# Performance work log

Measured on AMD Instinct MI355X. Metric: run time of the kernel, lower is better.

The kernel has to match this reference:

```python
import jax, jax.numpy as jnp
import numpy as np
from jax import lax

D_MODEL = 1024
D_INNER = 2048
B = 8
T = 2048
INIT_ALPHA_BIAS = 2.0


def setup_inputs() -> dict:
    key = jax.random.key(0)
    ks = jax.random.split(key, 6)
    def xavier(k, shape):
        fan_in, fan_out = shape[1], shape[0]
        lim = float(np.sqrt(6.0 / (fan_in + fan_out)))
        return jax.random.uniform(k, shape, jnp.float32, -lim, lim)
    return {
        "x": jax.random.normal(ks[0], (B, T, D_MODEL), jnp.float32),
        "h0": jnp.zeros((B, D_INNER), jnp.float32),
        "W_in": xavier(ks[1], (D_INNER, D_MODEL)),
        "W_alpha": xavier(ks[2], (D_INNER, D_INNER)),
        "b_alpha": jnp.full((D_INNER,), INIT_ALPHA_BIAS, jnp.float32),
        "W_v": xavier(ks[3], (D_INNER, D_INNER)),
        "b_v": jnp.zeros((D_INNER,), jnp.float32),
        "W_out": xavier(ks[4], (D_MODEL, D_INNER)),
    }


def reference(x, h0, W_in, W_alpha, b_alpha, W_v, b_v, W_out):
    # in_proj + silu pre-activation: [B,T,D_inner]
    x_proj = jax.nn.silu(jnp.einsum('btd,id->bti', x, W_in))
    # time-major for the scan: [T,B,D_inner]
    xr = jnp.transpose(x_proj, (1, 0, 2))
    # precompute gate and value for all steps (big GEMMs)
    alpha = jax.nn.sigmoid(jnp.einsum('tbd,ed->tbe', xr, W_alpha) + b_alpha)
    v = jnp.einsum('tbd,ed->tbe', xr, W_v) + b_v

    def step(h, av):
        a, vt = av
        h_new = a * h + (1.0 - a) * vt  # decay-gated update
        out_t = h_new * jax.nn.silu(h_new)  # self-gating
        return h_new, out_t

    h_final, outs = lax.scan(step, h0, (alpha, v))  # outs: [T,B,D_inner]
    # out_proj back to model dim, batch-major: [B,T,D_model]
    output = jnp.einsum('tbe,de->btd', outs, W_out)
    return output, h_final
```

## Files before the change

kernel.cpp:

```cpp
#include <hip/hip_runtime.h>
#include <cstdint>
#include <cstddef>

typedef unsigned short u16;
typedef unsigned int   u32;

#define D_MODEL 1024
#define D_INNER 2048
#define BATCH   8
#define TSEQ    2048
#define MROWS   (BATCH*TSEQ)
#define CHUNK   32
#define NCHUNK  (TSEQ/CHUNK)
#define EDIM    (BATCH*D_INNER)

typedef float  f32x4  __attribute__((ext_vector_type(4)));
typedef __bf16 bf16x8 __attribute__((ext_vector_type(8)));
typedef short  s16x8  __attribute__((ext_vector_type(8)));

__device__ __forceinline__ float bf2f(u16 u){ return __builtin_bit_cast(float, (u32)u << 16); }
__device__ __forceinline__ u16 f2bf(float f){
  u32 u = __builtin_bit_cast(u32, f);
  u += 0x7fffu + ((u >> 16) & 1u);
  return (u16)(u >> 16);
}
__device__ __forceinline__ float sigm(float x){ return 1.0f/(1.0f + __expf(-x)); }

__device__ __forceinline__ void gld16(const u16* g, u16* l){
  __builtin_amdgcn_global_load_lds((const __attribute__((address_space(1))) void*)g,
                                   (__attribute__((address_space(3))) void*)l, 16, 0, 0);
}

__device__ __forceinline__ s16x8 cvt8(const float* s){
  float4 u0 = *(const float4*)s;
  float4 u1 = *(const float4*)(s + 4);
  s16x8 p;
  p[0]=(short)f2bf(u0.x); p[1]=(short)f2bf(u0.y);
  p[2]=(short)f2bf(u0.z); p[3]=(short)f2bf(u0.w);
  p[4]=(short)f2bf(u1.x); p[5]=(short)f2bf(u1.y);
  p[6]=(short)f2bf(u1.z); p[7]=(short)f2bf(u1.w);
  return p;
}

#define LOADA(AF, MH) \
  _Pragma("unroll") \
  for (int mf = 0; mf < 4; ++mf){ \
    AF[mf][0] = *(const s16x8*)(As + (wr*128 + (MH)*64 + mf*16 + l15)*128 + csw); \
    AF[mf][1] = *(const s16x8*)(As + (wr*128 + (MH)*64 + mf*16 + l15)*128 + (csw^64)); \
  }
#define LOADB(BF, NH) \
  _Pragma("unroll") \
  for (int nf = 0; nf < 2; ++nf){ \
    BF[nf][0] = *(const s16x8*)(Bs + (wc*64 + (NH)*32 + nf*16 + l15)*128 + csw); \
    BF[nf][1] = *(const s16x8*)(Bs + (wc*64 + (NH)*32 + nf*16 + l15)*128 + (csw^64)); \
  }
#define MFMAQ(AF, BF, MH, NH) \
  __builtin_amdgcn_s_setprio(1); \
  _Pragma("unroll") \
  for (int mf = 0; mf < 4; ++mf) \
    _Pragma("unroll") \
    for (int nf = 0; nf < 2; ++nf) \
      _Pragma("unroll") \
      for (int ks = 0; ks < 2; ++ks) \
        acc[(MH)*4+mf][(NH)*2+nf] = __builtin_amdgcn_mfma_f32_16x16x32_bf16( \
            __builtin_bit_cast(bf16x8, AF[mf][ks]), \
            __builtin_bit_cast(bf16x8, BF[nf][ks]), \
            acc[(MH)*4+mf][(NH)*2+nf], 0, 0, 0); \
  __builtin_amdgcn_s_setprio(0);

template<int MODE, int K, int N>
__global__ __launch_bounds__(512, 2) void gemm256(
    const u16* __restrict__ A, const u16* __restrict__ Bt,
    const float* __restrict__ bias, const float* __restrict__ bias2,
    void* __restrict__ Cout, void* __restrict__ Cout2)
{
  __shared__ __align__(16) u16 sAB[2][2][16384];
  constexpr int NT = K/64;
  const int tid = threadIdx.x;
  const int w = tid >> 6, lane = tid & 63;
  const int wr = w >> 2, wc = w & 3;
  const int l15 = lane & 15, kg = lane >> 4;
  const int bm = blockIdx.x, bn = blockIdx.y;

  const int st_row  = w*8 + (lane>>3);
  const int st_cole = ((lane&7) ^ (lane>>3)) << 3;
  const size_t a_base = (size_t)(bm*256)*K + st_cole;
  const size_t b_base = (size_t)(bn*256)*K + st_cole;

  auto stageA = [&](int buf, int kt, int upper){
    u16* dst = &sAB[0][buf][upper*8192 + w*512];
    #pragma unroll
    for (int i = 0; i < 2; ++i)
      gld16(A + a_base + (size_t)(upper*128 + i*64 + st_row)*K + kt*64, dst + i*4096);
  };
  auto stageB = [&](int buf, int kt, int upper){
    u16* dst = &sAB[1][buf][upper*8192 + w*512];
    #pragma unroll
    for (int i = 0; i < 2; ++i)
      gld16(Bt + b_base + (size_t)(upper*128 + i*64 + st_row)*K + kt*64, dst + i*4096);
  };

  const int csw = (kg*16) ^ ((l15&7)<<4);

  f32x4 acc[8][4] = {};

  stageA(0,0,0); stageB(0,0,0); stageA(0,0,1); stageB(0,0,1);
  asm volatile("s_waitcnt vmcnt(0)" ::: "memory");
  __builtin_amdgcn_s_barrier();

  for (int t = 0; t < NT; ++t){
    const char* As = (const char*)&sAB[0][t&1][0];
    const char* Bs = (const char*)&sAB[1][t&1][0];
    const int nb = (t+1)&1;
    const bool more = (t < NT-1);
    s16x8 af[4][2], bf0[2][2], bf1[2][2];

    LOADA(af, 0)
    LOADB(bf0, 0)
    if (more){ stageA(nb, t+1, 0); stageA(nb, t+1, 1); }
    __builtin_amdgcn_s_barrier();
    MFMAQ(af, bf0, 0, 0)
    __builtin_amdgcn_s_barrier();

    LOADB(bf1, 1)
    if (more){ stageB(nb, t+1, 0); stageB(nb, t+1, 1); }
    __builtin_amdgcn_s_barrier();
    MFMAQ(af, bf1, 0, 1)
    __builtin_amdgcn_s_barrier();

    LOADA(af, 1)
    __builtin_amdgcn_s_barrier();
    MFMAQ(af, bf1, 1, 1)
    __builtin_amdgcn_s_barrier();

    asm volatile("s_waitcnt vmcnt(0)" ::: "memory");
    __builtin_amdgcn_s_barrier();
    MFMAQ(af, bf0, 1, 0)
    __builtin_amdgcn_s_barrier();
  }

  #pragma unroll
  for (int mi = 0; mi < 8; ++mi){
    #pragma unroll
    for (int ni = 0; ni < 4; ++ni){
      #pragma unroll
      for (int r = 0; r < 4; ++r){
        const int row = bm*256 + wr*128 + mi*16 + kg*4 + r;
        const int col = bn*256 + wc*64 + ni*16 + l15;
        float val = acc[mi][ni][r];
        if constexpr (MODE == 0){
          val = val * sigm(val);
          ((u16*)Cout)[(size_t)row*N + col] = f2bf(val);
        } else if constexpr (MODE == 3){
          const int orow = (row & 7)*TSEQ + (row >> 3);
          ((float*)Cout)[(size_t)orow*N + col] = val;
        } else if constexpr (MODE == 4){
          if (col < D_INNER){
            val = sigm(val + bias[col]);
            ((u16*)Cout)[(size_t)row*D_INNER + col] = f2bf(val);
          } else {
            val = val + bias2[col - D_INNER];
            ((u16*)Cout2)[(size_t)row*D_INNER + (col - D_INNER)] = f2bf(val);
          }
        }
      }
    }
  }
}

template<int MODE, int K, int N, bool BA, bool BB>
__global__ __launch_bounds__(256) void gemm_bt(
    const void* __restrict__ Ap, const void* __restrict__ Bp,
    const float* __restrict__ bias, void* __restrict__ Cout)
{
  __shared__ __align__(16) u16 sA[128*32];
  __shared__ __align__(16) u16 sB[128*32];
  const int tid = threadIdx.x;
  const int bm = blockIdx.x, bn = blockIdx.y;
  const int w = tid >> 6, lane = tid & 63;
  const int wr = w >> 1, wc = w & 1;
  const int l15 = lane & 15, kg = lane >> 4;
  const int r0   = tid >> 2;
  const int koff = (tid & 3) * 8;

  int ga[2];
  #pragma unroll
  for (int i = 0; i < 2; ++i){
    int mc = bm*128 + r0 + i*64;
    if (MODE == 0)      ga[i] = (mc & 7) * TSEQ + (mc >> 3);
    else if (MODE == 3) ga[i] = (mc & (TSEQ-1)) * BATCH + (mc >> 11);
    else                ga[i] = mc;
  }
  const u16*   Abf = (const u16*)Ap;
  const float* Af  = (const float*)Ap;
  const u16*   Bbf = (const u16*)Bp;
  const float* Bf  = (const float*)Bp;
  u16* la[2] = { sA + w*512, sA + 2048 + w*512 };
  u16* lb[2] = { sB + w*512, sB + 2048 + w*512 };
  u16* ldsA = sA + tid*8;
  u16* ldsB = sB + tid*8;
  const int gb[2] = { bn*128 + r0, bn*128 + r0 + 64 };

  f32x4 acc[4][4] = {};
  for (int kt = 0; kt < K/32; ++kt){
    __syncthreads();
    if constexpr (BA){
      gld16(Abf + (size_t)ga[0]*K + koff + kt*32, la[0]);
      gld16(Abf + (size_t)ga[1]*K + koff + kt*32, la[1]);
    } else {
      #pragma unroll
      for (int i = 0; i < 2; ++i)
        *(s16x8*)(ldsA + i*2048) = cvt8(Af + (size_t)ga[i]*K + koff + kt*32);
    }
    if constexpr (BB){
      gld16(Bbf + (size_t)gb[0]*K + koff + kt*32, lb[0]);
      gld16(Bbf + (size_t)gb[1]*K + koff + kt*32, lb[1]);
    } else {
      #pragma unroll
      for (int i = 0; i < 2; ++i)
        *(s16x8*)(ldsB + i*2048) = cvt8(Bf + (size_t)gb[i]*K + koff + kt*32);
    }
    __syncthreads();

    s16x8 af[4], bfr[4];
    #pragma unroll
    for (int m = 0; m < 4; ++m)
      af[m] = *(const s16x8*)(sA + (wr*64 + m*16 + l15)*32 + kg*8);
    #pragma unroll
    for (int n = 0; n < 4; ++n)
      bfr[n] = *(const s16x8*)(sB + (wc*64 + n*16 + l15)*32 + kg*8);
    #pragma unroll
    for (int m = 0; m < 4; ++m)
      #pragma unroll
      for (int n = 0; n < 4; ++n)
        acc[m][n] = __builtin_amdgcn_mfma_f32_16x16x32_bf16(
            __builtin_bit_cast(bf16x8, af[m]),
            __builtin_bit_cast(bf16x8, bfr[n]),
            acc[m][n], 0, 0, 0);
  }
  #pragma unroll
  for (int m = 0; m < 4; ++m)
    #pragma unroll
    for (int n = 0; n < 4; ++n)
      #pragma unroll
      for (int r = 0; r < 4; ++r){
        const int row = bm*128 + wr*64 + m*16 + kg*4 + r;
        const int col = bn*128 + wc*64 + n*16 + l15;
        float val = acc[m][n][r];
        if constexpr (MODE == 0){
          val = val * sigm(val);
          ((u16*)Cout)[(size_t)row*N + col] = f2bf(val);
        } else if constexpr (MODE == 1){
          val = sigm(val + bias[col]);
          ((u16*)Cout)[(size_t)row*N + col] = f2bf(val);
        } else if constexpr (MODE == 2){
          val = val + bias[col];
          ((u16*)Cout)[(size_t)row*N + col] = f2bf(val);
        } else {
          ((float*)Cout)[(size_t)row*N + col] = val;
        }
      }
}

__global__ __launch_bounds__(256) void scan_pass1(
    const u16* __restrict__ alpha, const u16* __restrict__ v,
    float* __restrict__ P, float* __restrict__ H)
{
  const int e = blockIdx.x*256 + threadIdx.x;
  const int c = blockIdx.y;
  const size_t base = (size_t)c*CHUNK*EDIM + e;
  float p = 1.f, h = 0.f;
  #pragma unroll 8
  for (int t = 0; t < CHUNK; ++t){
    float a  = bf2f(alpha[base + (size_t)t*EDIM]);
    float vv = bf2f(v[base + (size_t)t*EDIM]);
    p *= a;
    h = a*h + (1.f - a)*vv;
  }
  P[(size_t)c*EDIM + e] = p;
  H[(size_t)c*EDIM + e] = h;
}

__global__ __launch_bounds__(256) void scan_pass2(
    const float* __restrict__ P, const float* __restrict__ H,
    const float* __restrict__ h0, float* __restrict__ hstart,
    float* __restrict__ hfinal)
{
  const int e = blockIdx.x*256 + threadIdx.x;
  float hs = h0[e];
  for (int c = 0; c < NCHUNK; ++c){
    hstart[(size_t)c*EDIM + e] = hs;
    hs = P[(size_t)c*EDIM + e]*hs + H[(size_t)c*EDIM + e];
  }
  hfinal[e] = hs;
}

__global__ __launch_bounds__(256) void scan_pass3(
    const u16* __restrict__ alpha, const u16* __restrict__ v,
    const float* __restrict__ hstart, u16* __restrict__ outs)
{
  const int e = blockIdx.x*256 + threadIdx.x;
  const int c = blockIdx.y;
  const size_t base = (size_t)c*CHUNK*EDIM + e;
  float h = hstart[(size_t)c*EDIM + e];
  #pragma unroll 8
  for (int t = 0; t < CHUNK; ++t){
    float a  = bf2f(alpha[base + (size_t)t*EDIM]);
    float vv = bf2f(v[base + (size_t)t*EDIM]);
    h = a*h + (1.f - a)*vv;
    float o = h*h*sigm(h);
    outs[base + (size_t)t*EDIM] = f2bf(o);
  }
}

__global__ __launch_bounds__(256) void cvt_bf16(
    const float* __restrict__ src, u16* __restrict__ dst, int n4)
{
  const int i = blockIdx.x*256 + threadIdx.x;
  if (i >= n4) return;
  const float4 f = ((const float4*)src)[i];
  u32 w0 = (u32)f2bf(f.x) | ((u32)f2bf(f.y) << 16);
  u32 w1 = (u32)f2bf(f.z) | ((u32)f2bf(f.w) << 16);
  ((uint2*)dst)[i] = make_uint2(w0, w1);
}

__global__ __launch_bounds__(256) void cvt_x_tm(
    const float* __restrict__ src, u16* __restrict__ dst)
{
  const int i = blockIdx.x*256 + threadIdx.x;
  const int d4  = i & 255;
  const int rin = i >> 8;
  const int b = rin >> 11, tt = rin & (TSEQ-1);
  const int rout = tt*BATCH + b;
  const float4 f = ((const float4*)src)[i];
  u32 w0 = (u32)f2bf(f.x) | ((u32)f2bf(f.y) << 16);
  u32 w1 = (u32)f2bf(f.z) | ((u32)f2bf(f.w) << 16);
  ((uint2*)dst)[(size_t)rout*256 + d4] = make_uint2(w0, w1);
}

extern "C" void kernel_launch(void* const* d_in, const int* in_sizes, int n_in,
                              void* d_out, int out_size, void* d_ws, size_t ws_size,
                              hipStream_t stream)
{
  const float* x     = (const float*)d_in[0];
  const float* h0    = (const float*)d_in[1];
  const float* W_in  = (const float*)d_in[2];
  const float* W_al  = (const float*)d_in[3];
  const float* b_al  = (const float*)d_in[4];
  const float* W_v   = (const float*)d_in[5];
  const float* b_v   = (const float*)d_in[6];
  const float* W_out = (const float*)d_in[7];

  float* out  = (float*)d_out;
  float* hfin = out + (size_t)MROWS*D_MODEL;

  const size_t SZ_ACT = (size_t)MROWS*D_INNER*2;
  const size_t SZ_ST  = (size_t)NCHUNK*EDIM*4;
  const size_t SZ_WI  = (size_t)D_INNER*D_MODEL*2;
  const size_t SZ_WA  = (size_t)D_INNER*D_INNER*2;
  const size_t need_min  = 3*SZ_ACT + 3*SZ_ST;
  const size_t need_fast = need_min + 2*SZ_WI + 2*SZ_WA + 8192;

  if (ws_size < need_min) return;

  char* ws = (char*)d_ws;
  auto carve = [&](size_t bytes){
    char* p = ws; ws += (bytes + 255) & ~(size_t)255; return p;
  };
  u16* xp   = (u16*)carve(SZ_ACT);
  u16* alp  = (u16*)carve(SZ_ACT);
  u16* vv   = (u16*)carve(SZ_ACT);
  float* P  = (float*)carve(SZ_ST);
  float* H  = (float*)carve(SZ_ST);
  float* hs = (float*)carve(SZ_ST);

  const dim3 gScan(EDIM/256, NCHUNK);

  auto cvt = [&](const float* s, u16* d, size_t n){
    int n4 = (int)(n/4);
    cvt_bf16<<<(n4+255)/256, 256, 0, stream>>>(s, d, n4);
  };

  if (ws_size >= need_fast){
    u16* wib = (u16*)carve(SZ_WI);
    u16* wab = (u16*)carve(SZ_WA);
    u16* wvb = (u16*)carve(SZ_WA);
    u16* wob = (u16*)carve(SZ_WI);
    u16* xb  = alp;

    cvt_x_tm<<<(MROWS*D_MODEL/4)/256, 256, 0, stream>>>(x, xb);
    cvt(W_in,  wib, (size_t)D_INNER*D_MODEL);
    cvt(W_al,  wab, (size_t)D_INNER*D_INNER);
    cvt(W_v,   wvb, (size_t)D_INNER*D_INNER);
    cvt(W_out, wob, (size_t)D_MODEL*D_INNER);

    gemm256<0, D_MODEL, D_INNER><<<dim3(MROWS/256, D_INNER/256), 512, 0, stream>>>(
        xb, wib, nullptr, nullptr, xp, nullptr);
    gemm256<4, D_INNER, 2*D_INNER><<<dim3(MROWS/256, 2*D_INNER/256), 512, 0, stream>>>(
        xp, wab, b_al, b_v, alp, vv);

    scan_pass1<<<gScan, 256, 0, stream>>>(alp, vv, P, H);
    scan_pass2<<<EDIM/256, 256, 0, stream>>>(P, H, h0, hs, hfin);
    scan_pass3<<<gScan, 256, 0, stream>>>(alp, vv, hs, vv);

    gemm256<3, D_INNER, D_MODEL><<<dim3(MROWS/256, D_MODEL/256), 512, 0, stream>>>(
        vv, wob, nullptr, nullptr, out, nullptr);
  } else {
    const dim3 gBig(MROWS/128, D_INNER/128);
    const dim3 gOut(MROWS/128, D_MODEL/128);
    gemm_bt<0, D_MODEL, D_INNER, false, false><<<gBig, 256, 0, stream>>>(x,  W_in, nullptr, xp);
    gemm_bt<1, D_INNER, D_INNER, true,  false><<<gBig, 256, 0, stream>>>(xp, W_al, b_al,    alp);
    gemm_bt<2, D_INNER, D_INNER, true,  false><<<gBig, 256, 0, stream>>>(xp, W_v,  b_v,     vv);

    scan_pass1<<<gScan, 256, 0, stream>>>(alp, vv, P, H);
    scan_pass2<<<EDIM/256, 256, 0, stream>>>(P, H, h0, hs, hfin);
    scan_pass3<<<gScan, 256, 0, stream>>>(alp, vv, hs, vv);

    gemm_bt<3, D_INNER, D_MODEL, true, false><<<gOut, 256, 0, stream>>>(vv, W_out, nullptr, out);
  }
}
```

Baseline: 547.5 us.

## Reorder GEMM tile staging and use partial vmcnt waits for finer overlap

```diff
diff --git a/kernel.cpp b/kernel.cpp
--- a/kernel.cpp
+++ b/kernel.cpp
@@ -82,30 +82,35 @@
   const int l15 = lane & 15, kg = lane >> 4;
   const int bm = blockIdx.x, bn = blockIdx.y;
 
-  const int st_row  = w*8 + (lane>>3);
-  const int st_cole = ((lane&7) ^ (lane>>3)) << 3;
+  const int st_rw   = lane >> 3;
+  const int st_cole = ((lane&7) ^ st_rw) << 3;
   const size_t a_base = (size_t)(bm*256)*K + st_cole;
   const size_t b_base = (size_t)(bn*256)*K + st_cole;
 
-  auto stageA = [&](int buf, int kt, int upper){
-    u16* dst = &sAB[0][buf][upper*8192 + w*512];
-    #pragma unroll
-    for (int i = 0; i < 2; ++i)
-      gld16(A + a_base + (size_t)(upper*128 + i*64 + st_row)*K + kt*64, dst + i*4096);
+  auto stageA = [&](int buf, int kt, int set){
+    u16* dst = &sAB[0][buf][set*4096 + w*512];
+    #pragma unroll
+    for (int i = 0; i < 2; ++i){
+      const int row = set*64 + i*128 + w*8 + st_rw;
+      gld16(A + a_base + (size_t)row*K + kt*64, dst + i*8192);
+    }
   };
-  auto stageB = [&](int buf, int kt, int upper){
-    u16* dst = &sAB[1][buf][upper*8192 + w*512];
-    #pragma unroll
-    for (int i = 0; i < 2; ++i)
-      gld16(Bt + b_base + (size_t)(upper*128 + i*64 + st_row)*K + kt*64, dst + i*4096);
+  auto stageB = [&](int buf, int kt, int set){
+    #pragma unroll
+    for (int i = 0; i < 2; ++i){
+      const int g = i*64 + w*8;
+      const int rowbase = (g>>5)*64 + set*32 + (g&31);
+      gld16(Bt + b_base + (size_t)(rowbase + st_rw)*K + kt*64,
+            &sAB[1][buf][rowbase*64]);
+    }
   };
 
   const int csw = (kg*16) ^ ((l15&7)<<4);
 
   f32x4 acc[8][4] = {};
 
-  stageA(0,0,0); stageB(0,0,0); stageA(0,0,1); stageB(0,0,1);
-  asm volatile("s_waitcnt vmcnt(0)" ::: "memory");
+  stageB(0,0,0); stageA(0,0,0); stageB(0,0,1); stageA(0,0,1);
+  asm volatile("s_waitcnt vmcnt(4)" ::: "memory");
   __builtin_amdgcn_s_barrier();
 
   for (int t = 0; t < NT; ++t){
@@ -117,23 +122,36 @@
 
     LOADA(af, 0)
     LOADB(bf0, 0)
-    if (more){ stageA(nb, t+1, 0); stageA(nb, t+1, 1); }
+    if (more){
+      stageB(nb, t+1, 0); stageA(nb, t+1, 0);
+      asm volatile("s_waitcnt vmcnt(6)" ::: "memory");
+    } else {
+      asm volatile("s_waitcnt vmcnt(2)" ::: "memory");
+    }
     __builtin_amdgcn_s_barrier();
     MFMAQ(af, bf0, 0, 0)
     __builtin_amdgcn_s_barrier();
 
     LOADB(bf1, 1)
-    if (more){ stageB(nb, t+1, 0); stageB(nb, t+1, 1); }
+    if (more){
+      stageB(nb, t+1, 1);
+      asm volatile("s_waitcnt vmcnt(6)" ::: "memory");
+    } else {
+      asm volatile("s_waitcnt vmcnt(0)" ::: "memory");
+    }
     __builtin_amdgcn_s_barrier();
     MFMAQ(af, bf1, 0, 1)
     __builtin_amdgcn_s_barrier();
 
     LOADA(af, 1)
+    if (more){ stageA(nb, t+1, 1); }
     __builtin_amdgcn_s_barrier();
     MFMAQ(af, bf1, 1, 1)
     __builtin_amdgcn_s_barrier();
 
-    asm volatile("s_waitcnt vmcnt(0)" ::: "memory");
+    if (more){
+      asm volatile("s_waitcnt vmcnt(4)" ::: "memory");
+    }
     __builtin_amdgcn_s_barrier();
     MFMAQ(af, bf0, 1, 0)
     __builtin_amdgcn_s_barrier();
```

Measured after the change: 538.9 us. Within noise of the previous version (-1.6%).

## Restructure GEMM mainloop into 4-stage K=32 pipeline with register double-buffering

Applied to the files above, without the earlier changes.

```diff
diff --git a/kernel.cpp b/kernel.cpp
--- a/kernel.cpp
+++ b/kernel.cpp
@@ -42,31 +42,41 @@
   return p;
 }
 
-#define LOADA(AF, MH) \
+#define READR(AF, BF, RBUF) { \
+  const char* As_ = (const char*)&sAB[0][RBUF][0]; \
+  const char* Bs_ = (const char*)&sAB[1][RBUF][0]; \
   _Pragma("unroll") \
-  for (int mf = 0; mf < 4; ++mf){ \
-    AF[mf][0] = *(const s16x8*)(As + (wr*128 + (MH)*64 + mf*16 + l15)*128 + csw); \
-    AF[mf][1] = *(const s16x8*)(As + (wr*128 + (MH)*64 + mf*16 + l15)*128 + (csw^64)); \
-  }
-#define LOADB(BF, NH) \
+  for (int mi = 0; mi < 8; ++mi) \
+    AF[mi] = *(const s16x8*)(As_ + aoff + mi*1024); \
   _Pragma("unroll") \
-  for (int nf = 0; nf < 2; ++nf){ \
-    BF[nf][0] = *(const s16x8*)(Bs + (wc*64 + (NH)*32 + nf*16 + l15)*128 + csw); \
-    BF[nf][1] = *(const s16x8*)(Bs + (wc*64 + (NH)*32 + nf*16 + l15)*128 + (csw^64)); \
-  }
-#define MFMAQ(AF, BF, MH, NH) \
+  for (int ni = 0; ni < 4; ++ni) \
+    BF[ni] = *(const s16x8*)(Bs_ + boff + ni*1024); \
+}
+
+#define MFMAC(AF, BF) \
   __builtin_amdgcn_s_setprio(1); \
   _Pragma("unroll") \
-  for (int mf = 0; mf < 4; ++mf) \
+  for (int mi = 0; mi < 8; ++mi) \
     _Pragma("unroll") \
-    for (int nf = 0; nf < 2; ++nf) \
-      _Pragma("unroll") \
-      for (int ks = 0; ks < 2; ++ks) \
-        acc[(MH)*4+mf][(NH)*2+nf] = __builtin_amdgcn_mfma_f32_16x16x32_bf16( \
-            __builtin_bit_cast(bf16x8, AF[mf][ks]), \
-            __builtin_bit_cast(bf16x8, BF[nf][ks]), \
-            acc[(MH)*4+mf][(NH)*2+nf], 0, 0, 0); \
+    for (int ni = 0; ni < 4; ++ni) \
+      acc[mi][ni] = __builtin_amdgcn_mfma_f32_16x16x32_bf16( \
+          __builtin_bit_cast(bf16x8, AF[mi]), \
+          __builtin_bit_cast(bf16x8, BF[ni]), \
+          acc[mi][ni], 0, 0, 0); \
   __builtin_amdgcn_s_setprio(0);
+
+#define ITER(J, AC, BC, AN, BN, RBUF, SBUF) { \
+  if ((J) < NT-2) { asm volatile("s_waitcnt vmcnt(4)" ::: "memory"); } \
+  else            { asm volatile("s_waitcnt vmcnt(0)" ::: "memory"); } \
+  __builtin_amdgcn_s_barrier(); \
+  if ((J)+1 < NT) READR(AN, BN, RBUF) \
+  if ((J)+3 < NT) stage(SBUF, (J)+3); \
+  __builtin_amdgcn_sched_barrier(0); \
+  if ((J)+1 < NT) { asm volatile("s_waitcnt lgkmcnt(12)" ::: "memory"); } \
+  else            { asm volatile("s_waitcnt lgkmcnt(0)" ::: "memory"); } \
+  __builtin_amdgcn_sched_barrier(0); \
+  MFMAC(AC, BC) \
+}
 
 template<int MODE, int K, int N>
 __global__ __launch_bounds__(512, 2) void gemm256(
@@ -74,69 +84,44 @@
     const float* __restrict__ bias, const float* __restrict__ bias2,
     void* __restrict__ Cout, void* __restrict__ Cout2)
 {
-  __shared__ __align__(16) u16 sAB[2][2][16384];
-  constexpr int NT = K/64;
+  __shared__ __align__(16) u16 sAB[2][4][8192];
+  constexpr int NT = K/32;
   const int tid = threadIdx.x;
   const int w = tid >> 6, lane = tid & 63;
   const int wr = w >> 2, wc = w & 3;
   const int l15 = lane & 15, kg = lane >> 4;
   const int bm = blockIdx.x, bn = blockIdx.y;
 
-  const int st_row  = w*8 + (lane>>3);
-  const int st_cole = ((lane&7) ^ (lane>>3)) << 3;
-  const size_t a_base = (size_t)(bm*256)*K + st_cole;
-  const size_t b_base = (size_t)(bn*256)*K + st_cole;
-
-  auto stageA = [&](int buf, int kt, int upper){
-    u16* dst = &sAB[0][buf][upper*8192 + w*512];
-    #pragma unroll
-    for (int i = 0; i < 2; ++i)
-      gld16(A + a_base + (size_t)(upper*128 + i*64 + st_row)*K + kt*64, dst + i*4096);
+  const int st_r = w*16 + (lane>>2);
+  const int st_c = (lane&3)*8;
+  const u16* gA = A  + (size_t)(bm*256 + st_r)*K + st_c;
+  const u16* gB = Bt + (size_t)(bn*256 + st_r)*K + st_c;
+
+  auto stage = [&](int buf, int kt){
+    u16* dA = &sAB[0][buf][w*512];
+    u16* dB = &sAB[1][buf][w*512];
+    gld16(gA + (size_t)kt*32,             dA);
+    gld16(gA + (size_t)128*K + kt*32,     dA + 4096);
+    gld16(gB + (size_t)kt*32,             dB);
+    gld16(gB + (size_t)128*K + kt*32,     dB + 4096);
   };
-  auto stageB = [&](int buf, int kt, int upper){
-    u16* dst = &sAB[1][buf][upper*8192 + w*512];
-    #pragma unroll
-    for (int i = 0; i < 2; ++i)
-      gld16(Bt + b_base + (size_t)(upper*128 + i*64 + st_row)*K + kt*64, dst + i*4096);
-  };
-
-  const int csw = (kg*16) ^ ((l15&7)<<4);
-
+
+  const int aoff = (wr*128 + l15)*64 + kg*16;
+  const int boff = (wc*64  + l15)*64 + kg*16;
+
+  s16x8 aE[8], bE[4], aO[8], bO[4];
   f32x4 acc[8][4] = {};
 
-  stageA(0,0,0); stageB(0,0,0); stageA(0,0,1); stageB(0,0,1);
-  asm volatile("s_waitcnt vmcnt(0)" ::: "memory");
+  stage(0,0); stage(1,1); stage(2,2);
+  asm volatile("s_waitcnt vmcnt(8)" ::: "memory");
   __builtin_amdgcn_s_barrier();
-
-  for (int t = 0; t < NT; ++t){
-    const char* As = (const char*)&sAB[0][t&1][0];
-    const char* Bs = (const char*)&sAB[1][t&1][0];
-    const int nb = (t+1)&1;
-    const bool more = (t < NT-1);
-    s16x8 af[4][2], bf0[2][2], bf1[2][2];
-
-    LOADA(af, 0)
-    LOADB(bf0, 0)
-    if (more){ stageA(nb, t+1, 0); stageA(nb, t+1, 1); }
-    __builtin_amdgcn_s_barrier();
-    MFMAQ(af, bf0, 0, 0)
-    __builtin_amdgcn_s_barrier();
-
-    LOADB(bf1, 1)
-    if (more){ stageB(nb, t+1, 0); stageB(nb, t+1, 1); }
-    __builtin_amdgcn_s_barrier();
-    MFMAQ(af, bf1, 0, 1)
-    __builtin_amdgcn_s_barrier();
-
-    LOADA(af, 1)
-    __builtin_amdgcn_s_barrier();
-    MFMAQ(af, bf1, 1, 1)
-    __builtin_amdgcn_s_barrier();
-
-    asm volatile("s_waitcnt vmcnt(0)" ::: "memory");
-    __builtin_amdgcn_s_barrier();
-    MFMAQ(af, bf0, 1, 0)
-    __builtin_amdgcn_s_barrier();
+  READR(aE, bE, 0)
+
+  for (int j = 0; j < NT; j += 4){
+    ITER(j,   aE, bE, aO, bO, 1, 3)
+    ITER(j+1, aO, bO, aE, bE, 2, 0)
+    ITER(j+2, aE, bE, aO, bO, 3, 1)
+    ITER(j+3, aO, bO, aE, bE, 0, 2)
   }
 
   #pragma unroll
```

New measurement: 1.040 ms. 90.0% more time.
